# Kernel optimization log

Measured on AMD Instinct MI355X. Metric: run time of the kernel, lower is better.

The kernel has to match this reference:

```python
import jax, jax.numpy as jnp
import numpy as np
from jax import lax

FAN_IN = 16          # fixed number of parents per decoder node
THRESHOLD = 12       # node is active iff >= 12/16 parents are active
K_NODES = 1024       # decoders in this layer
M_PREV = 1024        # nodes in previous layer
N_SPATIAL = 64       # n x n output matrices


def setup_inputs() -> dict:
    key = jax.random.key(0)
    k1, k2, k3, k4, k5 = jax.random.split(key, 5)
    prev_outputs = jax.random.normal(k1, (M_PREV, N_SPATIAL, N_SPATIAL), dtype=jnp.float32)
    # Bernoulli(0.85) so the 12/16 threshold gate is genuinely data-dependent
    prev_is_active = jax.random.bernoulli(k2, 0.85, (M_PREV,))
    parent_indices = jax.random.randint(k3, (K_NODES, FAN_IN), 0, M_PREV, dtype=jnp.int32)
    # Per-node decoder params: 3x3 conv collapsing 16 parent channels -> 1 map, plus bias
    W = jax.random.normal(k4, (K_NODES, FAN_IN, 3, 3), dtype=jnp.float32) * 0.05
    b = jax.random.normal(k5, (K_NODES,), dtype=jnp.float32) * 0.05
    return {"prev_outputs": prev_outputs, "prev_is_active": prev_is_active,
            "parent_indices": parent_indices, "W": W, "b": b}


def reference(prev_outputs, prev_is_active, parent_indices, W, b):
    K, n = parent_indices.shape[0], prev_outputs.shape[-1]
    # Irregular static-wiring gather: (K, 16, n, n) and (K, 16)
    gathered = prev_outputs[parent_indices]
    gathered_flags = prev_is_active[parent_indices]
    # Threshold gate: node active iff >= 12 of its 16 parents are active
    out_active = jnp.sum(gathered_flags.astype(jnp.int32), axis=1) >= THRESHOLD  # (K,)
    # K independent 16->1 convs with distinct weights == one grouped conv (groups = K)
    x = gathered.reshape(1, K * FAN_IN, n, n)          # NCHW
    y = lax.conv_general_dilated(
        x, W, window_strides=(1, 1), padding='SAME',
        dimension_numbers=('NCHW', 'OIHW', 'NCHW'),
        feature_group_count=K,
    )[0]                                               # (K, n, n)
    y = jnp.tanh(y + b[:, None, None])
    # Inactive nodes emit a zero tensor
    out = jnp.where(out_active[:, None, None], y, jnp.zeros((), dtype=y.dtype))
    return out, out_active
```

## Files before the change

### kernel.cpp

```cpp
#include <hip/hip_runtime.h>

#define KN      1024
#define FAN_IN  16
#define NSP     64
#define THRESH  12

__device__ __forceinline__ float tanh_fast(float x) {
    float ax = fabsf(x);
    float e  = __expf(-2.0f * ax);
    float r  = 1.0f - 2.0f * e * __builtin_amdgcn_rcpf(1.0f + e);
    return copysignf(r, x);
}

__device__ __forceinline__ float dpp_shr1(float x) {
    return __int_as_float(__builtin_amdgcn_update_dpp(
        0, __float_as_int(x), 0x111, 0xF, 0xF, true));
}
__device__ __forceinline__ float dpp_shl1(float x) {
    return __int_as_float(__builtin_amdgcn_update_dpp(
        0, __float_as_int(x), 0x101, 0xF, 0xF, true));
}

__global__ __launch_bounds__(256) void decoder_kernel(
    const float* __restrict__ prev_outputs,
    const void*  __restrict__ prev_is_active,
    const int*   __restrict__ parent_indices,
    const float* __restrict__ Wt,
    const float* __restrict__ bias,
    float*       __restrict__ out)
{
    const int bid  = blockIdx.x;
    const int k    = bid >> 1;
    const int half = bid & 1;
    const int tid  = threadIdx.x;
    const int cg   = tid & 15;
    const int rp   = half * 16 + (tid >> 4);
    const int c0   = cg * 4;
    const int rA   = 2 * rp;

    bool bytemode = false;
    {
        const unsigned* sv = (const unsigned*)prev_is_active;
        #pragma unroll
        for (int i = 0; i < 16; ++i)
            if (sv[i] > 1u) bytemode = true;
    }

    const int* pidx = parent_indices + k * FAN_IN;
    int cnt = 0;
    #pragma unroll
    for (int i = 0; i < FAN_IN; ++i) {
        int p = pidx[i];
        int f;
        if (bytemode) f = (((const unsigned char*)prev_is_active)[p] != 0);
        else          f = (((const int*)prev_is_active)[p] != 0);
        cnt += f;
    }
    const bool active = (cnt >= THRESH);

    const size_t obase = (size_t)k * (NSP * NSP);
    if (half == 0 && tid == 0)
        out[(size_t)KN * NSP * NSP + k] = active ? 1.0f : 0.0f;

    if (!active) {
        float4 z = make_float4(0.f, 0.f, 0.f, 0.f);
        float4* o4 = (float4*)(out + obase + (size_t)half * 32 * NSP);
        o4[tid]       = z;
        o4[tid + 256] = z;
        return;
    }

    const float mL = (cg > 0)  ? 1.0f : 0.0f;
    const float mR = (cg < 15) ? 1.0f : 0.0f;
    const float mT = (rp > 0)  ? 1.0f : 0.0f;
    const float mB = (rp < 31) ? 1.0f : 0.0f;
    const int   gr0 = (rp > 0)  ? rA - 1 : 0;
    const int   gr3 = (rp < 31) ? rA + 2 : 63;

    const float* wbase = Wt + (size_t)k * FAN_IN * 9;

    float acc[8];
    #pragma unroll
    for (int s = 0; s < 8; ++s) acc[s] = 0.0f;

#define ROW_FMA(base, W0, W1, W2)                                              \
    acc[(base)+0] = fmaf(W0, l,   fmaf(W1, m.x, fmaf(W2, m.y, acc[(base)+0])));\
    acc[(base)+1] = fmaf(W0, m.x, fmaf(W1, m.y, fmaf(W2, m.z, acc[(base)+1])));\
    acc[(base)+2] = fmaf(W0, m.y, fmaf(W1, m.z, fmaf(W2, m.w, acc[(base)+2])));\
    acc[(base)+3] = fmaf(W0, m.z, fmaf(W1, m.w, fmaf(W2, r,   acc[(base)+3])));

    for (int ch = 0; ch < FAN_IN; ++ch) {
        const int p = pidx[ch];
        const float* __restrict__ src = prev_outputs + (size_t)p * (NSP * NSP);

        const float4 v0 = *(const float4*)(src + gr0      * NSP + c0);
        const float4 v1 = *(const float4*)(src + rA       * NSP + c0);
        const float4 v2 = *(const float4*)(src + (rA + 1) * NSP + c0);
        const float4 v3 = *(const float4*)(src + gr3      * NSP + c0);

        const float* w = wbase + ch * 9;
        const float wl0 = w[0], wc0 = w[1], wr0 = w[2];
        const float wl1 = w[3], wc1 = w[4], wr1 = w[5];
        const float wl2 = w[6], wc2 = w[7], wr2 = w[8];

        float4 m; float l, r;

        m = v0; l = dpp_shr1(m.w) * mL; r = dpp_shl1(m.x) * mR;
        m.x *= mT; m.y *= mT; m.z *= mT; m.w *= mT; l *= mT; r *= mT;
        ROW_FMA(0, wl0, wc0, wr0);

        m = v1; l = dpp_shr1(m.w) * mL; r = dpp_shl1(m.x) * mR;
        ROW_FMA(0, wl1, wc1, wr1);
        ROW_FMA(4, wl0, wc0, wr0);

        m = v2; l = dpp_shr1(m.w) * mL; r = dpp_shl1(m.x) * mR;
        ROW_FMA(0, wl2, wc2, wr2);
        ROW_FMA(4, wl1, wc1, wr1);

        m = v3; l = dpp_shr1(m.w) * mL; r = dpp_shl1(m.x) * mR;
        m.x *= mB; m.y *= mB; m.z *= mB; m.w *= mB; l *= mB; r *= mB;
        ROW_FMA(4, wl2, wc2, wr2);
    }
#undef ROW_FMA

    const float bk = bias[k];
    float4 o0, o1;
    o0.x = tanh_fast(acc[0] + bk); o0.y = tanh_fast(acc[1] + bk);
    o0.z = tanh_fast(acc[2] + bk); o0.w = tanh_fast(acc[3] + bk);
    o1.x = tanh_fast(acc[4] + bk); o1.y = tanh_fast(acc[5] + bk);
    o1.z = tanh_fast(acc[6] + bk); o1.w = tanh_fast(acc[7] + bk);
    *(float4*)(out + obase + (size_t)rA       * NSP + c0) = o0;
    *(float4*)(out + obase + (size_t)(rA + 1) * NSP + c0) = o1;
}

extern "C" void kernel_launch(void* const* d_in, const int* in_sizes, int n_in,
                              void* d_out, int out_size, void* d_ws, size_t ws_size,
                              hipStream_t stream) {
    const float* prev_outputs   = (const float*)d_in[0];
    const void*  prev_is_active = d_in[1];
    const int*   parent_indices = (const int*)d_in[2];
    const float* Wt             = (const float*)d_in[3];
    const float* bias           = (const float*)d_in[4];
    float*       out            = (float*)d_out;

    decoder_kernel<<<dim3(KN * 2), dim3(256), 0, stream>>>(
        prev_outputs, prev_is_active, parent_indices, Wt, bias, out);
}
```

Baseline: 39.49 us.

## Stage parent maps into LDS via async global_load_lds with double buffering

Each block now handles one whole decoder node with 512 threads. Every 64x64 parent map is copied into a double-buffered LDS tile using global_load_lds, so the load of the next channel overlaps compute on the current one. Each wave computes 8 rows with one column per lane, using wavefront-wide DPP shifts to get horizontal neighbours. This drops the redundant halo-row global loads and gives long contiguous copies, but adds a __syncthreads per channel and uses 32KB of LDS per block, which may limit occupancy.

```diff
diff --git a/kernel.cpp b/kernel.cpp
--- a/kernel.cpp
+++ b/kernel.cpp
@@ -12,16 +12,23 @@
     return copysignf(r, x);
 }
 
-__device__ __forceinline__ float dpp_shr1(float x) {
+__device__ __forceinline__ float dpp_wshr1(float x) {
     return __int_as_float(__builtin_amdgcn_update_dpp(
-        0, __float_as_int(x), 0x111, 0xF, 0xF, true));
+        0, __float_as_int(x), 0x138, 0xF, 0xF, true));
 }
-__device__ __forceinline__ float dpp_shl1(float x) {
+__device__ __forceinline__ float dpp_wshl1(float x) {
     return __int_as_float(__builtin_amdgcn_update_dpp(
-        0, __float_as_int(x), 0x101, 0xF, 0xF, true));
+        0, __float_as_int(x), 0x130, 0xF, 0xF, true));
 }
 
-__global__ __launch_bounds__(256) void decoder_kernel(
+__device__ __forceinline__ void gload_lds16(const float* g, float* l) {
+    __builtin_amdgcn_global_load_lds(
+        (const __attribute__((address_space(1))) unsigned*)g,
+        (__attribute__((address_space(3)))       unsigned*)l,
+        16, 0, 0);
+}
+
+__global__ __launch_bounds__(512, 8) void decoder_kernel(
     const float* __restrict__ prev_outputs,
     const void*  __restrict__ prev_is_active,
     const int*   __restrict__ parent_indices,
@@ -29,14 +36,13 @@
     const float* __restrict__ bias,
     float*       __restrict__ out)
 {
-    const int bid  = blockIdx.x;
-    const int k    = bid >> 1;
-    const int half = bid & 1;
+    __shared__ float sbuf[2][NSP * NSP];
+
+    const int k    = blockIdx.x;
     const int tid  = threadIdx.x;
-    const int cg   = tid & 15;
-    const int rp   = half * 16 + (tid >> 4);
-    const int c0   = cg * 4;
-    const int rA   = 2 * rp;
+    const int lane = tid & 63;
+    const int wv   = tid >> 6;
+    const int r0   = wv * 8;
 
     bool bytemode = false;
     {
@@ -59,23 +65,21 @@
     const bool active = (cnt >= THRESH);
 
     const size_t obase = (size_t)k * (NSP * NSP);
-    if (half == 0 && tid == 0)
+    if (tid == 0)
         out[(size_t)KN * NSP * NSP + k] = active ? 1.0f : 0.0f;
 
     if (!active) {
         float4 z = make_float4(0.f, 0.f, 0.f, 0.f);
-        float4* o4 = (float4*)(out + obase + (size_t)half * 32 * NSP);
+        float4* o4 = (float4*)(out + obase);
         o4[tid]       = z;
-        o4[tid + 256] = z;
+        o4[tid + 512] = z;
         return;
     }
 
-    const float mL = (cg > 0)  ? 1.0f : 0.0f;
-    const float mR = (cg < 15) ? 1.0f : 0.0f;
-    const float mT = (rp > 0)  ? 1.0f : 0.0f;
-    const float mB = (rp < 31) ? 1.0f : 0.0f;
-    const int   gr0 = (rp > 0)  ? rA - 1 : 0;
-    const int   gr3 = (rp < 31) ? rA + 2 : 63;
+    const float mT = (wv > 0) ? 1.0f : 0.0f;
+    const float mB = (wv < 7) ? 1.0f : 0.0f;
+    const int   rT = (wv > 0) ? r0 - 1 : 0;
+    const int   rB = (wv < 7) ? r0 + 8 : 63;
 
     const float* wbase = Wt + (size_t)k * FAN_IN * 9;
 
@@ -83,54 +87,51 @@
     #pragma unroll
     for (int s = 0; s < 8; ++s) acc[s] = 0.0f;
 
-#define ROW_FMA(base, W0, W1, W2)                                              \
-    acc[(base)+0] = fmaf(W0, l,   fmaf(W1, m.x, fmaf(W2, m.y, acc[(base)+0])));\
-    acc[(base)+1] = fmaf(W0, m.x, fmaf(W1, m.y, fmaf(W2, m.z, acc[(base)+1])));\
-    acc[(base)+2] = fmaf(W0, m.y, fmaf(W1, m.z, fmaf(W2, m.w, acc[(base)+2])));\
-    acc[(base)+3] = fmaf(W0, m.z, fmaf(W1, m.w, fmaf(W2, r,   acc[(base)+3])));
+#define STAGE(buf, p)                                                         \
+    {                                                                         \
+        const float* g = prev_outputs + (size_t)(p) * (NSP * NSP);            \
+        gload_lds16(g + tid * 4,        &sbuf[buf][wv * 256]);                \
+        gload_lds16(g + 2048 + tid * 4, &sbuf[buf][2048 + wv * 256]);         \
+    }
 
+    STAGE(0, pidx[0]);
+    __syncthreads();
+
+    #pragma unroll 2
     for (int ch = 0; ch < FAN_IN; ++ch) {
-        const int p = pidx[ch];
-        const float* __restrict__ src = prev_outputs + (size_t)p * (NSP * NSP);
+        if (ch + 1 < FAN_IN) STAGE((ch + 1) & 1, pidx[ch + 1]);
 
-        const float4 v0 = *(const float4*)(src + gr0      * NSP + c0);
-        const float4 v1 = *(const float4*)(src + rA       * NSP + c0);
-        const float4 v2 = *(const float4*)(src + (rA + 1) * NSP + c0);
-        const float4 v3 = *(const float4*)(src + gr3      * NSP + c0);
-
-        const float* w = wbase + ch * 9;
+        const float* sb = sbuf[ch & 1];
+        const float* w  = wbase + ch * 9;
         const float wl0 = w[0], wc0 = w[1], wr0 = w[2];
         const float wl1 = w[3], wc1 = w[4], wr1 = w[5];
         const float wl2 = w[6], wc2 = w[7], wr2 = w[8];
 
-        float4 m; float l, r;
+        float v[10], l[10], r[10];
+        v[0] = sb[rT * NSP + lane] * mT;
+        #pragma unroll
+        for (int j = 1; j <= 8; ++j) v[j] = sb[(r0 - 1 + j) * NSP + lane];
+        v[9] = sb[rB * NSP + lane] * mB;
+        #pragma unroll
+        for (int j = 0; j < 10; ++j) { l[j] = dpp_wshr1(v[j]); r[j] = dpp_wshl1(v[j]); }
 
-        m = v0; l = dpp_shr1(m.w) * mL; r = dpp_shl1(m.x) * mR;
-        m.x *= mT; m.y *= mT; m.z *= mT; m.w *= mT; l *= mT; r *= mT;
-        ROW_FMA(0, wl0, wc0, wr0);
+        #pragma unroll
+        for (int s = 0; s < 8; ++s) {
+            float a = acc[s];
+            a = fmaf(wl0, l[s],     fmaf(wc0, v[s],     fmaf(wr0, r[s],     a)));
+            a = fmaf(wl1, l[s + 1], fmaf(wc1, v[s + 1], fmaf(wr1, r[s + 1], a)));
+            a = fmaf(wl2, l[s + 2], fmaf(wc2, v[s + 2], fmaf(wr2, r[s + 2], a)));
+            acc[s] = a;
+        }
 
-        m = v1; l = dpp_shr1(m.w) * mL; r = dpp_shl1(m.x) * mR;
-        ROW_FMA(0, wl1, wc1, wr1);
-        ROW_FMA(4, wl0, wc0, wr0);
-
-        m = v2; l = dpp_shr1(m.w) * mL; r = dpp_shl1(m.x) * mR;
-        ROW_FMA(0, wl2, wc2, wr2);
-        ROW_FMA(4, wl1, wc1, wr1);
-
-        m = v3; l = dpp_shr1(m.w) * mL; r = dpp_shl1(m.x) * mR;
-        m.x *= mB; m.y *= mB; m.z *= mB; m.w *= mB; l *= mB; r *= mB;
-        ROW_FMA(4, wl2, wc2, wr2);
+        if (ch + 1 < FAN_IN) __syncthreads();
     }
-#undef ROW_FMA
+#undef STAGE
 
     const float bk = bias[k];
-    float4 o0, o1;
-    o0.x = tanh_fast(acc[0] + bk); o0.y = tanh_fast(acc[1] + bk);
-    o0.z = tanh_fast(acc[2] + bk); o0.w = tanh_fast(acc[3] + bk);
-    o1.x = tanh_fast(acc[4] + bk); o1.y = tanh_fast(acc[5] + bk);
-    o1.z = tanh_fast(acc[6] + bk); o1.w = tanh_fast(acc[7] + bk);
-    *(float4*)(out + obase + (size_t)rA       * NSP + c0) = o0;
-    *(float4*)(out + obase + (size_t)(rA + 1) * NSP + c0) = o1;
+    #pragma unroll
+    for (int s = 0; s < 8; ++s)
+        out[obase + (size_t)(r0 + s) * NSP + lane] = tanh_fast(acc[s] + bk);
 }
 
 extern "C" void kernel_launch(void* const* d_in, const int* in_sizes, int n_in,
@@ -143,6 +144,6 @@
     const float* bias           = (const float*)d_in[4];
     float*       out            = (float*)d_out;
 
-    decoder_kernel<<<dim3(KN * 2), dim3(256), 0, stream>>>(
+    decoder_kernel<<<dim3(KN), dim3(512), 0, stream>>>(
         prev_outputs, prev_is_active, parent_indices, Wt, bias, out);
 }
```

Result: no change. 39.10 us (-1.0%).
